# Kernel optimization log

Measured on AMD Instinct MI355X. Metric: run time of the kernel, lower is better.

## Reference

```python
import jax, jax.numpy as jnp
import numpy as np

N_NODES = 50000
N_EDGES = 1_600_000
NUM_GRAPHS = 64
F_NODE = 32
F_EDGE = 16
H = 64
L = 3
BN_EPS = 1e-5


def setup_inputs() -> dict:
    key = jax.random.key(0)
    ks = jax.random.split(key, 20)
    x = jax.random.normal(ks[0], (N_NODES, F_NODE), jnp.float32)
    edge_attr = jax.random.normal(ks[1], (N_EDGES, F_EDGE), jnp.float32)
    edge_index = jax.random.randint(ks[2], (2, N_EDGES), 0, N_NODES, dtype=jnp.int64)
    batch = jnp.sort(jax.random.randint(ks[3], (N_NODES,), 0, NUM_GRAPHS, dtype=jnp.int64))

    def lin(k, fan_in, shape):
        return jax.random.normal(k, shape, jnp.float32) * (1.0 / np.sqrt(fan_in))

    node_W = lin(ks[4], F_NODE, (F_NODE, H));  node_b = jnp.zeros((H,), jnp.float32)
    edge_W = lin(ks[5], F_EDGE, (F_EDGE, H));  edge_b = jnp.zeros((H,), jnp.float32)
    # GINE per-layer MLP: Linear(H, 2H) -> ReLU -> Linear(2H, H)
    W1s = lin(ks[6], H, (L, H, 2 * H));   b1s = jnp.zeros((L, 2 * H), jnp.float32)
    W2s = lin(ks[7], 2 * H, (L, 2 * H, H)); b2s = jnp.zeros((L, H), jnp.float32)
    gammas = jnp.ones((L, H), jnp.float32)
    betas = jnp.zeros((L, H), jnp.float32)
    lin_W = lin(ks[8], H, (H, 1));  lin_b = jnp.zeros((1,), jnp.float32)
    return {
        "x": x, "edge_attr": edge_attr, "edge_index": edge_index, "batch": batch,
        "node_W": node_W, "node_b": node_b, "edge_W": edge_W, "edge_b": edge_b,
        "W1s": W1s, "b1s": b1s, "W2s": W2s, "b2s": b2s,
        "gammas": gammas, "betas": betas, "lin_W": lin_W, "lin_b": lin_b,
    }


def reference(x, edge_attr, edge_index, batch, node_W, node_b, edge_W, edge_b,
              W1s, b1s, W2s, b2s, gammas, betas, lin_W, lin_b):
    # node / edge embeddings
    h = x @ node_W + node_b                  # [N, H]
    e = edge_attr @ edge_W + edge_b          # [E, H]
    src, dst = edge_index[0], edge_index[1]
    for l in range(L):
        # GINEConv (eps=0): m_ij = relu(x_j + e_ij), aggregate sum at target
        m = jax.nn.relu(h[src] + e)                                  # [E, H]
        agg = jax.ops.segment_sum(m, dst, num_segments=N_NODES)     # [N, H]
        z = h + agg
        z = jax.nn.relu(z @ W1s[l] + b1s[l]) @ W2s[l] + b2s[l]       # GINE MLP
        # BatchNorm (training-mode batch stats, biased variance) + ReLU
        mu = jnp.mean(z, axis=0)
        var = jnp.var(z, axis=0)
        h = jax.nn.relu(gammas[l] * (z - mu) * jax.lax.rsqrt(var + BN_EPS) + betas[l])
    # global mean pool per graph
    counts = jax.ops.segment_sum(jnp.ones((N_NODES,), h.dtype), batch, num_segments=NUM_GRAPHS)
    gsum = jax.ops.segment_sum(h, batch, num_segments=NUM_GRAPHS)   # [G, H]
    graph_x = gsum / jnp.maximum(counts, 1.0)[:, None]
    return graph_x @ lin_W + lin_b                                   # [G, 1]
```

## Files before the change

### kernel.cpp

```cpp
#include <hip/hip_runtime.h>

#define NN 50000
#define NE 1600000
#define NG 64
#define HD 64
#define BN_EPS 1e-5f
#define NTILES ((NN + 31) / 32)
#define NBUCK 8
#define NPB 6250
#define NBINS (NBUCK * NN)
#define NEP (NE + 512)
#define SLOTS 3584
#define CHUNK 2000
#define NCHUNK (NBINS / CHUNK)
#define CPB (NCHUNK / NBUCK)

typedef unsigned short ushort_t;
typedef unsigned int uint_t;
typedef __attribute__((ext_vector_type(8))) short bf16x8;
typedef __attribute__((ext_vector_type(4))) float f32x4;

__device__ __forceinline__ float b2f(ushort_t u) {
  union { uint_t i; float f; } v; v.i = ((uint_t)u) << 16; return v.f;
}
__device__ __forceinline__ ushort_t f2b(float f) {
  union { float f; uint_t i; } v; v.f = f;
  uint_t x = v.i;
  return (ushort_t)((x + 0x7fffu + ((x >> 16) & 1u)) >> 16);
}
__device__ __forceinline__ uint_t packsplit(float f) {
  ushort_t hi = f2b(f);
  float r = f - b2f(hi);
  ushort_t lo = f2b(r);
  return (uint_t)hi | ((uint_t)lo << 16);
}
__device__ __forceinline__ float LDF(const void* p, int i, int isb) {
  return isb ? b2f(((const ushort_t*)p)[i]) : ((const float*)p)[i];
}
__device__ __forceinline__ int LDI(const void* p, int i, int is64) {
  return is64 ? ((const int*)p)[2 * i] : ((const int*)p)[i];
}
__device__ __forceinline__ int clampi(int v, int hi) {
  return (v < 0) ? 0 : (v >= hi ? hi - 1 : v);
}

__global__ void detect_k(const uint_t* __restrict__ xw, const uint_t* __restrict__ ew,
                         int* __restrict__ flags) {
  int t = threadIdx.x;
  uint_t w = xw[t];
  uint_t b = (w >> 8) & 0x7fu;
  unsigned long long m1 = __ballot(b >= 0x3au && b <= 0x42u);
  unsigned long long m2 = __ballot(ew[2 * t + 1] == 0u);
  if (t == 0) {
    flags[0] = (__popcll(m1) >= 32) ? 1 : 0;
    flags[1] = (__popcll(m2) >= 56) ? 1 : 0;
  }
}

__global__ void __launch_bounds__(256) node_embed(
    const void* __restrict__ x, const void* __restrict__ W,
    const void* __restrict__ b, float* __restrict__ h, const int* __restrict__ flags) {
  __shared__ float xs[64 * 32];
  int isb = flags[0];
  int t = threadIdx.x;
  int base = blockIdx.x * 64;
  int nodes = NN - base; if (nodes > 64) nodes = 64;
  int idx = t * 8;
  if (idx < nodes * 32) {
    if (isb) {
      const uint4* p = (const uint4*)((const ushort_t*)x + base * 32);
      uint4 u = p[t];
      ushort_t* pu = (ushort_t*)&u;
      #pragma unroll
      for (int q = 0; q < 8; q++) xs[idx + q] = b2f(pu[q]);
    } else {
      const float4* p = (const float4*)((const float*)x + base * 32);
      float4 a = p[2 * t], d = p[2 * t + 1];
      xs[idx + 0] = a.x; xs[idx + 1] = a.y; xs[idx + 2] = a.z; xs[idx + 3] = a.w;
      xs[idx + 4] = d.x; xs[idx + 5] = d.y; xs[idx + 6] = d.z; xs[idx + 7] = d.w;
    }
  }
  int c = t & 63, s0 = t >> 6;
  float w[32];
  #pragma unroll
  for (int k = 0; k < 32; k++) w[k] = LDF(W, k * 64 + c, isb);
  float bc = LDF(b, c, isb);
  __syncthreads();
  #pragma unroll 4
  for (int i = 0; i < 16; i++) {
    int slot = s0 * 16 + i;
    int node = base + slot;
    if (node < NN) {
      float acc = bc;
      #pragma unroll
      for (int k = 0; k < 32; k++) acc += xs[slot * 32 + k] * w[k];
      h[node * 64 + c] = acc;
    }
  }
}

__global__ void __launch_bounds__(256) hist_k(
    const void* __restrict__ eidx, int* __restrict__ hist, const int* __restrict__ flags) {
  int is64 = flags[1];
  int e = blockIdx.x * 256 + threadIdx.x;
  if (e >= NE) return;
  int d = clampi(LDI(eidx, NE + e, is64), NN);
  int s = clampi(LDI(eidx, e, is64), NN);
  int bin = (s / NPB) * NN + d;
  atomicAdd(&hist[bin], 1);
}

__global__ void __launch_bounds__(256) scan_a(
    const int* __restrict__ hist, int* __restrict__ csum) {
  __shared__ int red[256];
  int c = blockIdx.x, t = threadIdx.x;
  int s = 0;
  if (t < 250) {
    const int4* h4 = (const int4*)(hist + c * CHUNK) + t * 2;
    int4 a = h4[0], b = h4[1];
    s = a.x + a.y + a.z + a.w + b.x + b.y + b.z + b.w;
  }
  red[t] = s;
  __syncthreads();
  for (int d = 128; d > 0; d >>= 1) {
    if (t < d) red[t] += red[t + d];
    __syncthreads();
  }
  if (t == 0) csum[c] = red[0];
}

__global__ void __launch_bounds__(256) scan_b(
    const int* __restrict__ csum, int* __restrict__ cbase, int* __restrict__ meta) {
  __shared__ int sc[NCHUNK];
  __shared__ int sT[NBUCK];
  __shared__ int sA[NBUCK + 1];
  int t = threadIdx.x;
  if (t < NCHUNK) sc[t] = csum[t];
  __syncthreads();
  if (t < NBUCK) {
    int T = 0;
    for (int i = 0; i < CPB; i++) T += sc[t * CPB + i];
    sT[t] = T;
  }
  __syncthreads();
  if (t == 0) {
    int a = 0;
    for (int b = 0; b < NBUCK; b++) {
      sA[b] = a;
      meta[b] = a;
      meta[16 + b] = a + sT[b];
      a = (a + sT[b] + 63) & ~63;
    }
    meta[NBUCK] = a;
    sA[NBUCK] = a;
  }
  __syncthreads();
  if (t < NBUCK) {
    int run = sA[t];
    for (int i = 0; i < CPB; i++) { cbase[t * CPB + i] = run; run += sc[t * CPB + i]; }
  }
}

__global__ void __launch_bounds__(256) scan_c(
    const int* __restrict__ hist, const int* __restrict__ cbase,
    int* __restrict__ starts) {
  __shared__ int buf[256];
  int c = blockIdx.x, t = threadIdx.x;
  int4 a = {0, 0, 0, 0}, b = {0, 0, 0, 0};
  int s = 0;
  if (t < 250) {
    const int4* h4 = (const int4*)(hist + c * CHUNK) + t * 2;
    a = h4[0]; b = h4[1];
    s = a.x + a.y + a.z + a.w + b.x + b.y + b.z + b.w;
  }
  buf[t] = s;
  __syncthreads();
  for (int d = 1; d < 256; d <<= 1) {
    int x = (t >= d) ? buf[t - d] : 0;
    __syncthreads();
    buf[t] += x;
    __syncthreads();
  }
  if (t < 250) {
    int run = cbase[c] + buf[t] - s;
    int4 o1, o2;
    o1.x = run; run += a.x;
    o1.y = run; run += a.y;
    o1.z = run; run += a.z;
    o1.w = run; run += a.w;
    o2.x = run; run += b.x;
    o2.y = run; run += b.y;
    o2.z = run; run += b.z;
    o2.w = run; run += b.w;
    int4* s4 = (int4*)(starts + c * CHUNK) + t * 2;
    s4[0] = o1; s4[1] = o2;
  }
}

__global__ void pad_fill(const int* __restrict__ meta, int* __restrict__ perm,
                         int* __restrict__ psrc, int* __restrict__ pdst) {
  int t = threadIdx.x;
  for (int b = 0; b < NBUCK; b++) {
    int re = meta[16 + b], ae = meta[b + 1];
    for (int p = re + t; p < ae; p += 64) {
      perm[p] = 0; psrc[p] = 0; pdst[p] = NN;
    }
  }
}

__global__ void __launch_bounds__(256) scatter_k(
    const void* __restrict__ eidx, int* __restrict__ cursor,
    int* __restrict__ perm, int* __restrict__ psrc, int* __restrict__ pdst,
    const int* __restrict__ flags) {
  int is64 = flags[1];
  int e = blockIdx.x * 256 + threadIdx.x;
  if (e >= NE) return;
  int d = clampi(LDI(eidx, NE + e, is64), NN);
  int s = clampi(LDI(eidx, e, is64), NN);
  int bin = (s / NPB) * NN + d;
  int pos = atomicAdd(&cursor[bin], 1);
  perm[pos] = e;
  psrc[pos] = s;
  pdst[pos] = d;
}

__global__ void __launch_bounds__(256) pack_eattr(
    const void* __restrict__ eattr, const int* __restrict__ perm,
    ushort_t* __restrict__ phi, ushort_t* __restrict__ plo,
    const int* __restrict__ flags, const int* __restrict__ meta) {
  int isb = flags[0];
  int pos = blockIdx.x * 256 + threadIdx.x;
  if (pos >= meta[8]) return;
  int e = perm[pos];
  int tile = pos >> 4, r = pos & 15;
  union U8 { ushort_t s[8]; uint4 u; };
  if (isb) {
    const uint4* p = (const uint4*)((const ushort_t*)eattr + (size_t)e * 16);
    uint4 h0 = p[0], h1 = p[1];
    ((uint4*)phi)[tile * 32 + r] = h0;
    ((uint4*)phi)[tile * 32 + 16 + r] = h1;
  } else {
    const float4* p = (const float4*)((const float*)eattr + (size_t)e * 16);
    U8 hi[2], lo[2];
    #pragma unroll
    for (int q = 0; q < 4; q++) {
      float4 v = p[q];
      float vv[4] = {v.x, v.y, v.z, v.w};
      #pragma unroll
      for (int j = 0; j < 4; j++) {
        int idx = q * 4 + j;
        ushort_t hb = f2b(vv[j]);
        hi[idx >> 3].s[idx & 7] = hb;
        lo[idx >> 3].s[idx & 7] = f2b(vv[j] - b2f(hb));
      }
    }
    ((uint4*)phi)[tile * 32 + r] = hi[0].u;
    ((uint4*)phi)[tile * 32 + 16 + r] = hi[1].u;
    ((uint4*)plo)[tile * 32 + r] = lo[0].u;
    ((uint4*)plo)[tile * 32 + 16 + r] = lo[1].u;
  }
}

__global__ void __launch_bounds__(256) edge_mfma(
    const ushort_t* __restrict__ phi, const ushort_t* __restrict__ plo,
    const int* __restrict__ psrc, const int* __restrict__ pdst,
    const uint4* __restrict__ wfrag, const float* __restrict__ h,
    float* __restrict__ agg, const int* __restrict__ flags,
    const int* __restrict__ meta) {
  __shared__ float es[64 * 68];
  __shared__ int ss[64], sd[64];
  int A[9];
  #pragma unroll
  for (int b = 0; b < 9; b++) A[b] = meta[b];
  int maxcb = 0;
  #pragma unroll
  for (int b = 0; b < NBUCK; b++) {
    int cb = (A[b + 1] - A[b]) >> 6;
    maxcb = cb > maxcb ? cb : maxcb;
  }
  int chunk;
  if (maxcb <= SLOTS) {
    int xcd = blockIdx.x & 7, s = blockIdx.x >> 3;
    if (s >= ((A[xcd + 1] - A[xcd]) >> 6)) return;
    chunk = (A[xcd] >> 6) + s;
  } else {
    chunk = blockIdx.x;
    if (chunk * 64 >= A[8]) return;
  }
  int base = chunk * 64;
  int isb = flags[0];
  int t = threadIdx.x;
  if (t < 64) ss[t] = psrc[base + t];
  else if (t < 128) sd[t - 64] = pdst[base + t - 64];
  int w = t >> 6, lane = t & 63, kg = lane >> 4, cr = lane & 15;
  int tile = chunk * 4 + w;
  union FR { uint4 u; bf16x8 v; };
  FR ahi, alo;
  ahi.u = make_uint4(0u, 0u, 0u, 0u);
  alo.u = ahi.u;
  if (kg < 2) {
    ahi.u = ((const uint4*)phi)[tile * 32 + kg * 16 + cr];
    if (!isb) alo.u = ((const uint4*)plo)[tile * 32 + kg * 16 + cr];
  }
  f32x4 acc[4];
  #pragma unroll
  for (int nt = 0; nt < 4; nt++) acc[nt] = (f32x4){0.f, 0.f, 0.f, 0.f};
  #pragma unroll
  for (int nt = 0; nt < 4; nt++) {
    FR bh; bh.u = wfrag[nt * 64 + lane];
    acc[nt] = __builtin_amdgcn_mfma_f32_16x16x32_bf16(ahi.v, bh.v, acc[nt], 0, 0, 0);
    if (!isb) {
      FR bl; bl.u = wfrag[256 + nt * 64 + lane];
      acc[nt] = __builtin_amdgcn_mfma_f32_16x16x32_bf16(ahi.v, bl.v, acc[nt], 0, 0, 0);
      acc[nt] = __builtin_amdgcn_mfma_f32_16x16x32_bf16(alo.v, bh.v, acc[nt], 0, 0, 0);
    }
  }
  const float* ebias = (const float*)(wfrag + 512);
  #pragma unroll
  for (int nt = 0; nt < 4; nt++) {
    float bv = ebias[nt * 16 + cr];
    #pragma unroll
    for (int r = 0; r < 4; r++)
      es[(w * 16 + kg * 4 + r) * 68 + nt * 16 + cr] = acc[nt][r] + bv;
  }
  __syncthreads();
  int c = lane, s0 = w;
  float hv[16];
  #pragma unroll
  for (int i = 0; i < 16; i++)
    hv[i] = h[(size_t)ss[s0 * 16 + i] * 64 + c];
  float accr = 0.f;
  int cur = -1;
  #pragma unroll
  for (int i = 0; i < 16; i++) {
    int slot = s0 * 16 + i;
    int dn = sd[slot];
    float m = hv[i] + es[slot * 68 + c];
    m = m > 0.f ? m : 0.f;
    if (dn != cur) {
      if (cur >= 0 && cur < NN) atomicAdd(&agg[cur * 64 + c], accr);
      cur = dn; accr = 0.f;
    }
    accr += m;
  }
  if (cur >= 0 && cur < NN) atomicAdd(&agg[cur * 64 + c], accr);
}

__global__ void __launch_bounds__(256) edge_sorted(
    const void* __restrict__ eattr, const int* __restrict__ perm,
    const int* __restrict__ psrc, const int* __restrict__ pdst,
    const void* __restrict__ eW, const void* __restrict__ eb,
    const float* __restrict__ h, float* __restrict__ agg,
    const int* __restrict__ flags, const int* __restrict__ meta) {
  __shared__ float ea[64 * 16];
  __shared__ int ss[64], sd[64];
  int isb = flags[0];
  int t = threadIdx.x;
  int base = blockIdx.x * 64;
  if (base >= meta[8]) return;
  if (t < 64) ss[t] = psrc[base + t];
  else if (t < 128) sd[t - 64] = pdst[base + t - 64];
  {
    int slot = t >> 2, q = t & 3;
    int pe = perm[base + slot];
    if (isb) {
      const uint2* p = (const uint2*)((const ushort_t*)eattr + (size_t)pe * 16 + q * 4);
      uint2 u = *p;
      ea[slot * 16 + q * 4 + 0] = b2f((ushort_t)(u.x & 0xffffu));
      ea[slot * 16 + q * 4 + 1] = b2f((ushort_t)(u.x >> 16));
      ea[slot * 16 + q * 4 + 2] = b2f((ushort_t)(u.y & 0xffffu));
      ea[slot * 16 + q * 4 + 3] = b2f((ushort_t)(u.y >> 16));
    } else {
      const float4* p = (const float4*)((const float*)eattr + (size_t)pe * 16 + q * 4);
      float4 v = *p;
      ea[slot * 16 + q * 4 + 0] = v.x;
      ea[slot * 16 + q * 4 + 1] = v.y;
      ea[slot * 16 + q * 4 + 2] = v.z;
      ea[slot * 16 + q * 4 + 3] = v.w;
    }
  }
  int c = t & 63, s0 = t >> 6;
  float w[16];
  #pragma unroll
  for (int k = 0; k < 16; k++) w[k] = LDF(eW, k * 64 + c, isb);
  float bc = LDF(eb, c, isb);
  __syncthreads();
  float acc = 0.f;
  int cur = -1;
  for (int i = 0; i < 16; i++) {
    int slot = s0 * 16 + i;
    int sn = ss[slot], dn = sd[slot];
    float e = bc;
    #pragma unroll
    for (int k = 0; k < 16; k++) e += ea[slot * 16 + k] * w[k];
    float m = h[sn * 64 + c] + e;
    m = m > 0.f ? m : 0.f;
    if (dn != cur) {
      if (cur >= 0 && cur < NN) atomicAdd(&agg[cur * 64 + c], acc);
      cur = dn; acc = 0.f;
    }
    acc += m;
  }
  if (cur >= 0 && cur < NN) atomicAdd(&agg[cur * 64 + c], acc);
}

__global__ void __launch_bounds__(256) prep_w(
    const void* __restrict__ W1s, const void* __restrict__ W2s,
    const void* __restrict__ eW, const void* __restrict__ eB,
    uint4* __restrict__ wpk, const int* __restrict__ flags) {
  int l = blockIdx.x, t = threadIdx.x, isb = flags[0];
  union U8 { ushort_t s[8]; uint4 u; };
  if (l == 3) {
    uint4* wfrag = wpk + 3 * 4096;
    int nt = t >> 6, lane = t & 63;
    int col = nt * 16 + (lane & 15);
    U8 hi, lo;
    #pragma unroll
    for (int j = 0; j < 8; j++) {
      int k = (lane >> 4) * 8 + j;
      float wf = (k < 16) ? LDF(eW, k * 64 + col, isb) : 0.f;
      ushort_t hb = f2b(wf);
      hi.s[j] = hb;
      lo.s[j] = f2b(wf - b2f(hb));
    }
    wfrag[nt * 64 + lane] = hi.u;
    wfrag[256 + nt * 64 + lane] = lo.u;
    if (t < 64) ((float*)(wfrag + 512))[t] = LDF(eB, t, isb);
    return;
  }
  uint4* w1hi = wpk + (size_t)l * 4096;
  uint4* w1lo = w1hi + 1024;
  uint4* w2hi = w1hi + 2048;
  uint4* w2lo = w1hi + 3072;
  for (int o = t; o < 1024; o += 256) {
    int lane = o & 63, f = (o >> 6) & 7, hh = o >> 9;
    int q = lane >> 4, m = lane & 15;
    {
      int kc = f >> 2, i = f & 3;
      U8 hi, lo;
      #pragma unroll
      for (int j = 0; j < 8; j++) {
        int idx = l * 8192 + (kc * 32 + q * 8 + j) * 128 + (hh * 4 + i) * 16 + m;
        float wf = LDF(W1s, idx, isb);
        ushort_t hb = f2b(wf);
        hi.s[j] = hb;
        lo.s[j] = f2b(wf - b2f(hb));
      }
      w1hi[o] = hi.u;
      w1lo[o] = lo.u;
    }
    {
      int kc = f >> 1, i = f & 1;
      U8 hi, lo;
      #pragma unroll
      for (int j = 0; j < 8; j++) {
        int idx = l * 8192 + (kc * 32 + q * 8 + j) * 64 + (hh * 2 + i) * 16 + m;
        float wf = LDF(W2s, idx, isb);
        ushort_t hb = f2b(wf);
        hi.s[j] = hb;
        lo.s[j] = f2b(wf - b2f(hb));
      }
      w2hi[o] = hi.u;
      w2lo[o] = lo.u;
    }
  }
}

__global__ void __launch_bounds__(256) mlp_mfma(
    const float* __restrict__ h, const float* agg,
    const uint4* __restrict__ wpk, const void* __restrict__ b1s,
    const void* __restrict__ b2s,
    float* z2out, float* __restrict__ bnsum, const int* __restrict__ flags, int layer) {
  __shared__ uint_t zs[32 * 65];
  __shared__ uint_t a1s[32 * 129];
  int isb = flags[0];
  int t = threadIdx.x;
  int w = t >> 6, lane = t & 63, q = lane >> 4, m = lane & 15;
  int mt = w & 1;
  int hh = w >> 1;
  int ng1 = hh * 4;
  int ng2 = hh * 2;
  int b1off = layer * 128, b2off = layer * 64;
  const uint4* w1hi = wpk + (size_t)layer * 4096;
  const uint4* w1lo = w1hi + 1024;
  const uint4* w2hi = w1hi + 2048;
  const uint4* w2lo = w1hi + 3072;

  union FR { uint4 u; bf16x8 v; };
  FR w1f[4][2], w2f[2][4];
  #pragma unroll
  for (int kc = 0; kc < 2; kc++)
    #pragma unroll
    for (int i = 0; i < 4; i++)
      w1f[i][kc].u = w1hi[(hh * 8 + kc * 4 + i) * 64 + lane];
  #pragma unroll
  for (int kc = 0; kc < 4; kc++)
    #pragma unroll
    for (int i = 0; i < 2; i++)
      w2f[i][kc].u = w2hi[(hh * 8 + kc * 2 + i) * 64 + lane];

  float b1v[4], b2v[2];
  #pragma unroll
  for (int i = 0; i < 4; i++) b1v[i] = LDF(b1s, b1off + (ng1 + i) * 16 + m, isb);
  #pragma unroll
  for (int i = 0; i < 2; i++) b2v[i] = LDF(b2s, b2off + (ng2 + i) * 16 + m, isb);

  int srow = t >> 3, scol = (t & 7) * 8;
  float ps[2] = {0.f, 0.f}, pq[2] = {0.f, 0.f};

  for (int tile = blockIdx.x; tile < NTILES; tile += gridDim.x) {
    int base = tile * 32;
    __syncthreads();
    {
      int gr = base + srow;
      if (gr < NN) {
        const float4* hp = (const float4*)(h + (size_t)gr * 64 + scol);
        const float4* ap = (const float4*)(agg + (size_t)gr * 64 + scol);
        float4 h0 = hp[0], h1 = hp[1], a0 = ap[0], a1 = ap[1];
        zs[srow * 65 + scol + 0] = packsplit(h0.x + a0.x);
        zs[srow * 65 + scol + 1] = packsplit(h0.y + a0.y);
        zs[srow * 65 + scol + 2] = packsplit(h0.z + a0.z);
        zs[srow * 65 + scol + 3] = packsplit(h0.w + a0.w);
        zs[srow * 65 + scol + 4] = packsplit(h1.x + a1.x);
        zs[srow * 65 + scol + 5] = packsplit(h1.y + a1.y);
        zs[srow * 65 + scol + 6] = packsplit(h1.z + a1.z);
        zs[srow * 65 + scol + 7] = packsplit(h1.w + a1.w);
      } else {
        #pragma unroll
        for (int jj = 0; jj < 8; jj++) zs[srow * 65 + scol + jj] = 0;
      }
    }
    __syncthreads();
    f32x4 acc1[4];
    #pragma unroll
    for (int i = 0; i < 4; i++) acc1[i] = (f32x4){0.f, 0.f, 0.f, 0.f};
    #pragma unroll
    for (int kc = 0; kc < 2; kc++) {
      int ab = (mt * 16 + m) * 65 + kc * 32 + q * 8;
      bf16x8 ahi, alo;
      #pragma unroll
      for (int j = 0; j < 8; j++) {
        uint_t u = zs[ab + j];
        ahi[j] = (short)(u & 0xffffu);
        alo[j] = (short)(u >> 16);
      }
      #pragma unroll
      for (int i = 0; i < 4; i++) {
        acc1[i] = __builtin_amdgcn_mfma_f32_16x16x32_bf16(ahi, w1f[i][kc].v, acc1[i], 0, 0, 0);
        acc1[i] = __builtin_amdgcn_mfma_f32_16x16x32_bf16(alo, w1f[i][kc].v, acc1[i], 0, 0, 0);
        if (!isb) {
          FR bl;
          bl.u = w1lo[(hh * 8 + kc * 4 + i) * 64 + lane];
          acc1[i] = __builtin_amdgcn_mfma_f32_16x16x32_bf16(ahi, bl.v, acc1[i], 0, 0, 0);
        }
      }
    }
    #pragma unroll
    for (int i = 0; i < 4; i++) {
      #pragma unroll
      for (int r = 0; r < 4; r++) {
        float v = acc1[i][r] + b1v[i];
        v = v > 0.f ? v : 0.f;
        a1s[(mt * 16 + q * 4 + r) * 129 + (ng1 + i) * 16 + m] = packsplit(v);
      }
    }
    __syncthreads();
    f32x4 acc2[2];
    #pragma unroll
    for (int i = 0; i < 2; i++) acc2[i] = (f32x4){0.f, 0.f, 0.f, 0.f};
    #pragma unroll
    for (int kc = 0; kc < 4; kc++) {
      int ab = (mt * 16 + m) * 129 + kc * 32 + q * 8;
      bf16x8 ahi, alo;
      #pragma unroll
      for (int j = 0; j < 8; j++) {
        uint_t u = a1s[ab + j];
        ahi[j] = (short)(u & 0xffffu);
        alo[j] = (short)(u >> 16);
      }
      #pragma unroll
      for (int i = 0; i < 2; i++) {
        acc2[i] = __builtin_amdgcn_mfma_f32_16x16x32_bf16(ahi, w2f[i][kc].v, acc2[i], 0, 0, 0);
        acc2[i] = __builtin_amdgcn_mfma_f32_16x16x32_bf16(alo, w2f[i][kc].v, acc2[i], 0, 0, 0);
        if (!isb) {
          FR bl;
          bl.u = w2lo[(hh * 8 + kc * 2 + i) * 64 + lane];
          acc2[i] = __builtin_amdgcn_mfma_f32_16x16x32_bf16(ahi, bl.v, acc2[i], 0, 0, 0);
        }
      }
    }
    #pragma unroll
    for (int i = 0; i < 2; i++) {
      int col = (ng2 + i) * 16 + m;
      #pragma unroll
      for (int r = 0; r < 4; r++) {
        int gr = base + mt * 16 + q * 4 + r;
        if (gr < NN) {
          float v = acc2[i][r] + b2v[i];
          z2out[(size_t)gr * 64 + col] = v;
          ps[i] += v; pq[i] += v * v;
        }
      }
    }
  }
  __syncthreads();
  float* red = (float*)zs;
  if (t < 128) red[t] = 0.f;
  __syncthreads();
  #pragma unroll
  for (int i = 0; i < 2; i++) {
    int col = (ng2 + i) * 16 + m;
    atomicAdd(&red[col], ps[i]);
    atomicAdd(&red[64 + col], pq[i]);
  }
  __syncthreads();
  if (t < 128) atomicAdd(&bnsum[t], red[t]);
}

__global__ void bn_fin(const float* __restrict__ bnsum, const void* __restrict__ gammas,
                       const void* __restrict__ betas, float* __restrict__ scsh,
                       const int* __restrict__ flags, int layer) {
  int c = threadIdx.x;
  int isb = flags[0];
  float inv_n = 1.0f / (float)NN;
  float mu = bnsum[c] * inv_n;
  float var = bnsum[64 + c] * inv_n - mu * mu;
  var = var > 0.f ? var : 0.f;
  float sc = LDF(gammas, layer * 64 + c, isb) * rsqrtf(var + BN_EPS);
  scsh[c] = sc;
  scsh[64 + c] = LDF(betas, layer * 64 + c, isb) - mu * sc;
}

__global__ void __launch_bounds__(256) bn_apply(
    const float* __restrict__ z2, const float* __restrict__ scsh, float* __restrict__ h) {
  int t = blockIdx.x * 256 + threadIdx.x;
  if (t < NN * 16) {
    float4 z = ((const float4*)z2)[t];
    int c4 = t & 15;
    float4 sc = ((const float4*)scsh)[c4];
    float4 sh = ((const float4*)(scsh + 64))[c4];
    float4 r;
    r.x = fmaxf(z.x * sc.x + sh.x, 0.f);
    r.y = fmaxf(z.y * sc.y + sh.y, 0.f);
    r.z = fmaxf(z.z * sc.z + sh.z, 0.f);
    r.w = fmaxf(z.w * sc.w + sh.w, 0.f);
    ((float4*)h)[t] = r;
  }
}

__global__ void __launch_bounds__(256) find_bounds(
    const void* __restrict__ batch, int* __restrict__ bounds, const int* __restrict__ flags) {
  int is64 = flags[1];
  int i = blockIdx.x * 256 + threadIdx.x;
  if (i >= NN) return;
  int cur = clampi(LDI(batch, i, is64), NG);
  if (i == 0) {
    for (int g = 0; g <= cur; g++) bounds[g] = 0;
  } else {
    int prev = clampi(LDI(batch, i - 1, is64), NG);
    for (int g = prev + 1; g <= cur; g++) bounds[g] = i;
  }
  if (i == NN - 1) {
    for (int g = cur + 1; g <= NG; g++) bounds[g] = NN;
  }
}

__global__ void __launch_bounds__(256) pool_final(
    const float* __restrict__ h, const int* __restrict__ bounds,
    const void* __restrict__ linW, const void* __restrict__ linB,
    float* __restrict__ out, const int* __restrict__ flags) {
  __shared__ float red[4][64];
  int isb = flags[0];
  int g = blockIdx.x;
  int t = threadIdx.x, c = t & 63, w = t >> 6;
  int s = bounds[g], e = bounds[g + 1];
  float acc = 0.f;
  for (int i = s + w; i < e; i += 4) acc += h[i * 64 + c];
  red[w][c] = acc;
  __syncthreads();
  if (t < 64) {
    float v = red[0][c] + red[1][c] + red[2][c] + red[3][c];
    float cnt = (float)(e - s); if (cnt < 1.f) cnt = 1.f;
    v = (v / cnt) * LDF(linW, c, isb);
    #pragma unroll
    for (int m = 32; m >= 1; m >>= 1) v += __shfl_xor(v, m, 64);
    if (c == 0) out[g] = v + LDF(linB, 0, isb);
  }
}

extern "C" void kernel_launch(void* const* d_in, const int* in_sizes, int n_in,
                              void* d_out, int out_size, void* d_ws, size_t ws_size,
                              hipStream_t stream) {
  const void* x     = d_in[0];
  const void* eattr = d_in[1];
  const void* eidx  = d_in[2];
  const void* batch = d_in[3];
  const void* nodeW = d_in[4];
  const void* nodeB = d_in[5];
  const void* edgeW = d_in[6];
  const void* edgeB = d_in[7];
  const void* W1s   = d_in[8];
  const void* b1s   = d_in[9];
  const void* W2s   = d_in[10];
  const void* b2s   = d_in[11];
  const void* gam   = d_in[12];
  const void* bet   = d_in[13];
  const void* linW  = d_in[14];
  const void* linB  = d_in[15];
  float* out = (float*)d_out;

  int*   flags  = (int*)d_ws;
  int*   meta   = flags + 16;
  float* h      = (float*)(meta + 48);
  float* agg    = h + (size_t)NN * HD;
  float* bnsum  = agg + (size_t)NN * HD;
  float* scsh   = bnsum + 128;
  int*   bounds = (int*)(scsh + 128);
  int*   csum   = bounds + 80;
  int*   cbase  = csum + NCHUNK;
  int*   offs   = cbase + NCHUNK;
  int*   cursor = offs + NBINS;
  int*   perm   = cursor + NBINS;
  int*   psrc   = perm + NEP;
  int*   pdst   = psrc + NEP;

  size_t base_words = 64ull + 2ull * NN * HD + 128 + 128 + 80
                    + 2ull * NCHUNK + 2ull * NBINS + 3ull * NEP;
  size_t wpk_words_start = (base_words + 3ull) & ~3ull;
  size_t wpk_words = (3ull * 4096 + 528) * 4;
  size_t needed = (wpk_words_start + wpk_words) * 4ull;
  if (ws_size < needed) return;
  uint4* wpk = (uint4*)((float*)d_ws + wpk_words_start);
  uint4* wfrag = wpk + 3ull * 4096;
  size_t z2_start = wpk_words_start + wpk_words;
  float* z2sep = (float*)d_ws + z2_start;
  int have_z2 = ws_size >= (z2_start + (size_t)NN * HD) * 4ull;
  float* z2 = have_z2 ? z2sep : agg;
  size_t pat_start = z2_start + (size_t)NN * HD;
  size_t pat_words = (size_t)NEP * 8;
  int have_pat = have_z2 && (ws_size >= (pat_start + 2ull * pat_words) * 4ull);
  ushort_t* phi = (ushort_t*)((float*)d_ws + pat_start);
  ushort_t* plo = (ushort_t*)((float*)d_ws + pat_start + pat_words);

  detect_k<<<1, 64, 0, stream>>>((const uint_t*)x, (const uint_t*)eidx, flags);
  prep_w<<<4, 256, 0, stream>>>(W1s, W2s, edgeW, edgeB, wpk, flags);
  node_embed<<<(NN + 63) / 64, 256, 0, stream>>>(x, nodeW, nodeB, h, flags);

  hipMemsetAsync(offs, 0, (size_t)NBINS * sizeof(int), stream);
  hist_k<<<NE / 256, 256, 0, stream>>>(eidx, offs, flags);
  scan_a<<<NCHUNK, 256, 0, stream>>>(offs, csum);
  scan_b<<<1, 256, 0, stream>>>(csum, cbase, meta);
  scan_c<<<NCHUNK, 256, 0, stream>>>(offs, cbase, cursor);
  pad_fill<<<1, 64, 0, stream>>>(meta, perm, psrc, pdst);
  scatter_k<<<NE / 256, 256, 0, stream>>>(eidx, cursor, perm, psrc, pdst, flags);
  if (have_pat)
    pack_eattr<<<NEP / 256, 256, 0, stream>>>(eattr, perm, phi, plo, flags, meta);

  for (int l = 0; l < 3; l++) {
    hipMemsetAsync(agg, 0, (size_t)NN * HD * sizeof(float), stream);
    if (have_pat)
      edge_mfma<<<8 * SLOTS, 256, 0, stream>>>(phi, plo, psrc, pdst, wfrag, h, agg, flags, meta);
    else
      edge_sorted<<<NEP / 64, 256, 0, stream>>>(eattr, perm, psrc, pdst, edgeW, edgeB, h, agg, flags, meta);
    hipMemsetAsync(bnsum, 0, 128 * sizeof(int), stream);
    mlp_mfma<<<784, 256, 0, stream>>>(h, agg, wpk, b1s, b2s, z2, bnsum, flags, l);
    bn_fin<<<1, 64, 0, stream>>>(bnsum, gam, bet, scsh, flags, l);
    bn_apply<<<3125, 256, 0, stream>>>(z2, scsh, h);
  }
  find_bounds<<<(NN + 255) / 256, 256, 0, stream>>>(batch, bounds, flags);
  pool_final<<<NG, 256, 0, stream>>>(h, bounds, linW, linB, out, flags);
}
```

Baseline: 948.8 us.

## Bin edges by destination block then source bucket for 64 sub-buckets

Measured after the change: 995.8 us. 4.9% more time.

```diff
diff --git a/kernel.cpp b/kernel.cpp
--- a/kernel.cpp
+++ b/kernel.cpp
@@ -8,12 +8,10 @@
 #define NTILES ((NN + 31) / 32)
 #define NBUCK 8
 #define NPB 6250
-#define NBINS (NBUCK * NN)
-#define NEP (NE + 512)
+#define NSB 64
+#define NBINS (NSB * NPB)
+#define NEP (NE + 4096)
 #define SLOTS 3584
-#define CHUNK 2000
-#define NCHUNK (NBINS / CHUNK)
-#define CPB (NCHUNK / NBUCK)
 
 typedef unsigned short ushort_t;
 typedef unsigned int uint_t;
@@ -106,19 +104,20 @@
   if (e >= NE) return;
   int d = clampi(LDI(eidx, NE + e, is64), NN);
   int s = clampi(LDI(eidx, e, is64), NN);
-  int bin = (s / NPB) * NN + d;
+  int bd = d / NPB, bs = s / NPB;
+  int bin = (bd * 8 + bs) * NPB + (d - bd * NPB);
   atomicAdd(&hist[bin], 1);
 }
 
 __global__ void __launch_bounds__(256) scan_a(
     const int* __restrict__ hist, int* __restrict__ csum) {
   __shared__ int red[256];
-  int c = blockIdx.x, t = threadIdx.x;
+  int sb = blockIdx.x, t = threadIdx.x;
   int s = 0;
   if (t < 250) {
-    const int4* h4 = (const int4*)(hist + c * CHUNK) + t * 2;
-    int4 a = h4[0], b = h4[1];
-    s = a.x + a.y + a.z + a.w + b.x + b.y + b.z + b.w;
+    const int* p = hist + sb * NPB + t * 25;
+    #pragma unroll 5
+    for (int i = 0; i < 25; i++) s += p[i];
   }
   red[t] = s;
   __syncthreads();
@@ -126,52 +125,35 @@
     if (t < d) red[t] += red[t + d];
     __syncthreads();
   }
-  if (t == 0) csum[c] = red[0];
-}
-
-__global__ void __launch_bounds__(256) scan_b(
-    const int* __restrict__ csum, int* __restrict__ cbase, int* __restrict__ meta) {
-  __shared__ int sc[NCHUNK];
-  __shared__ int sT[NBUCK];
-  __shared__ int sA[NBUCK + 1];
-  int t = threadIdx.x;
-  if (t < NCHUNK) sc[t] = csum[t];
-  __syncthreads();
-  if (t < NBUCK) {
-    int T = 0;
-    for (int i = 0; i < CPB; i++) T += sc[t * CPB + i];
-    sT[t] = T;
-  }
-  __syncthreads();
-  if (t == 0) {
+  if (t == 0) csum[sb] = red[0];
+}
+
+__global__ void scan_b(const int* __restrict__ csum, int* __restrict__ meta) {
+  if (threadIdx.x == 0) {
     int a = 0;
-    for (int b = 0; b < NBUCK; b++) {
-      sA[b] = a;
-      meta[b] = a;
-      meta[16 + b] = a + sT[b];
-      a = (a + sT[b] + 63) & ~63;
-    }
-    meta[NBUCK] = a;
-    sA[NBUCK] = a;
-  }
-  __syncthreads();
-  if (t < NBUCK) {
-    int run = sA[t];
-    for (int i = 0; i < CPB; i++) { cbase[t * CPB + i] = run; run += sc[t * CPB + i]; }
+    for (int sb = 0; sb < NSB; sb++) {
+      meta[sb] = a;
+      int T = csum[sb];
+      meta[128 + sb] = a + T;
+      a = (a + T + 63) & ~63;
+    }
+    meta[64] = a;
+    for (int x = 0; x < 8; x++) meta[96 + x] = meta[x * 8];
+    meta[96 + 8] = a;
   }
 }
 
 __global__ void __launch_bounds__(256) scan_c(
-    const int* __restrict__ hist, const int* __restrict__ cbase,
+    const int* __restrict__ hist, const int* __restrict__ meta,
     int* __restrict__ starts) {
   __shared__ int buf[256];
-  int c = blockIdx.x, t = threadIdx.x;
-  int4 a = {0, 0, 0, 0}, b = {0, 0, 0, 0};
+  int sb = blockIdx.x, t = threadIdx.x;
+  int loc[25];
   int s = 0;
   if (t < 250) {
-    const int4* h4 = (const int4*)(hist + c * CHUNK) + t * 2;
-    a = h4[0]; b = h4[1];
-    s = a.x + a.y + a.z + a.w + b.x + b.y + b.z + b.w;
+    const int* p = hist + sb * NPB + t * 25;
+    #pragma unroll 5
+    for (int i = 0; i < 25; i++) { loc[i] = p[i]; s += loc[i]; }
   }
   buf[t] = s;
   __syncthreads();
@@ -182,26 +164,19 @@
     __syncthreads();
   }
   if (t < 250) {
-    int run = cbase[c] + buf[t] - s;
-    int4 o1, o2;
-    o1.x = run; run += a.x;
-    o1.y = run; run += a.y;
-    o1.z = run; run += a.z;
-    o1.w = run; run += a.w;
-    o2.x = run; run += b.x;
-    o2.y = run; run += b.y;
-    o2.z = run; run += b.z;
-    o2.w = run; run += b.w;
-    int4* s4 = (int4*)(starts + c * CHUNK) + t * 2;
-    s4[0] = o1; s4[1] = o2;
+    int run = meta[sb] + buf[t] - s;
+    int* q = starts + sb * NPB + t * 25;
+    #pragma unroll 5
+    for (int i = 0; i < 25; i++) { q[i] = run; run += loc[i]; }
   }
 }
 
 __global__ void pad_fill(const int* __restrict__ meta, int* __restrict__ perm,
                          int* __restrict__ psrc, int* __restrict__ pdst) {
   int t = threadIdx.x;
-  for (int b = 0; b < NBUCK; b++) {
-    int re = meta[16 + b], ae = meta[b + 1];
+  for (int sb = 0; sb < NSB; sb++) {
+    int re = meta[128 + sb];
+    int ae = (sb < NSB - 1) ? meta[sb + 1] : meta[64];
     for (int p = re + t; p < ae; p += 64) {
       perm[p] = 0; psrc[p] = 0; pdst[p] = NN;
     }
@@ -217,7 +192,8 @@
   if (e >= NE) return;
   int d = clampi(LDI(eidx, NE + e, is64), NN);
   int s = clampi(LDI(eidx, e, is64), NN);
-  int bin = (s / NPB) * NN + d;
+  int bd = d / NPB, bs = s / NPB;
+  int bin = (bd * 8 + bs) * NPB + (d - bd * NPB);
   int pos = atomicAdd(&cursor[bin], 1);
   perm[pos] = e;
   psrc[pos] = s;
@@ -230,7 +206,7 @@
     const int* __restrict__ flags, const int* __restrict__ meta) {
   int isb = flags[0];
   int pos = blockIdx.x * 256 + threadIdx.x;
-  if (pos >= meta[8]) return;
+  if (pos >= meta[64]) return;
   int e = perm[pos];
   int tile = pos >> 4, r = pos & 15;
   union U8 { ushort_t s[8]; uint4 u; };
@@ -271,10 +247,10 @@
   __shared__ int ss[64], sd[64];
   int A[9];
   #pragma unroll
-  for (int b = 0; b < 9; b++) A[b] = meta[b];
+  for (int b = 0; b < 9; b++) A[b] = meta[96 + b];
   int maxcb = 0;
   #pragma unroll
-  for (int b = 0; b < NBUCK; b++) {
+  for (int b = 0; b < 8; b++) {
     int cb = (A[b + 1] - A[b]) >> 6;
     maxcb = cb > maxcb ? cb : maxcb;
   }
@@ -357,7 +333,7 @@
   int isb = flags[0];
   int t = threadIdx.x;
   int base = blockIdx.x * 64;
-  if (base >= meta[8]) return;
+  if (base >= meta[64]) return;
   if (t < 64) ss[t] = psrc[base + t];
   else if (t < 128) sd[t - 64] = pdst[base + t - 64];
   {
@@ -711,21 +687,20 @@
 
   int*   flags  = (int*)d_ws;
   int*   meta   = flags + 16;
-  float* h      = (float*)(meta + 48);
+  float* h      = (float*)(meta + 192);
   float* agg    = h + (size_t)NN * HD;
   float* bnsum  = agg + (size_t)NN * HD;
   float* scsh   = bnsum + 128;
   int*   bounds = (int*)(scsh + 128);
   int*   csum   = bounds + 80;
-  int*   cbase  = csum + NCHUNK;
-  int*   offs   = cbase + NCHUNK;
+  int*   offs   = csum + NSB;
   int*   cursor = offs + NBINS;
   int*   perm   = cursor + NBINS;
   int*   psrc   = perm + NEP;
   int*   pdst   = psrc + NEP;
 
-  size_t base_words = 64ull + 2ull * NN * HD + 128 + 128 + 80
-                    + 2ull * NCHUNK + 2ull * NBINS + 3ull * NEP;
+  size_t base_words = 16ull + 192 + 2ull * NN * HD + 128 + 128 + 80
+                    + NSB + 2ull * NBINS + 3ull * NEP;
   size_t wpk_words_start = (base_words + 3ull) & ~3ull;
   size_t wpk_words = (3ull * 4096 + 528) * 4;
   size_t needed = (wpk_words_start + wpk_words) * 4ull;
@@ -748,9 +723,9 @@
 
   hipMemsetAsync(offs, 0, (size_t)NBINS * sizeof(int), stream);
   hist_k<<<NE / 256, 256, 0, stream>>>(eidx, offs, flags);
-  scan_a<<<NCHUNK, 256, 0, stream>>>(offs, csum);
-  scan_b<<<1, 256, 0, stream>>>(csum, cbase, meta);
-  scan_c<<<NCHUNK, 256, 0, stream>>>(offs, cbase, cursor);
+  scan_a<<<NSB, 256, 0, stream>>>(offs, csum);
+  scan_b<<<1, 64, 0, stream>>>(csum, meta);
+  scan_c<<<NSB, 256, 0, stream>>>(offs, meta, cursor);
   pad_fill<<<1, 64, 0, stream>>>(meta, perm, psrc, pdst);
   scatter_k<<<NE / 256, 256, 0, stream>>>(eidx, cursor, perm, psrc, pdst, flags);
   if (have_pat)
```

## Process 128 edges per block with per-wave LDS and shuffle-based indices

Applied to the files above, without the earlier changes.

New measurement: 912.3 us. 1.04x faster.

```diff
diff --git a/kernel.cpp b/kernel.cpp
--- a/kernel.cpp
+++ b/kernel.cpp
@@ -9,8 +9,8 @@
 #define NBUCK 8
 #define NPB 6250
 #define NBINS (NBUCK * NN)
-#define NEP (NE + 512)
-#define SLOTS 3584
+#define NEP (NE + 2048)
+#define SLOTS 1792
 #define CHUNK 2000
 #define NCHUNK (NBINS / CHUNK)
 #define CPB (NCHUNK / NBUCK)
@@ -149,7 +149,7 @@
       sA[b] = a;
       meta[b] = a;
       meta[16 + b] = a + sT[b];
-      a = (a + sT[b] + 63) & ~63;
+      a = (a + sT[b] + 127) & ~127;
     }
     meta[NBUCK] = a;
     sA[NBUCK] = a;
@@ -267,81 +267,94 @@
     const uint4* __restrict__ wfrag, const float* __restrict__ h,
     float* __restrict__ agg, const int* __restrict__ flags,
     const int* __restrict__ meta) {
-  __shared__ float es[64 * 68];
-  __shared__ int ss[64], sd[64];
+  __shared__ float es[4][16 * 68];
   int A[9];
   #pragma unroll
   for (int b = 0; b < 9; b++) A[b] = meta[b];
   int maxcb = 0;
   #pragma unroll
   for (int b = 0; b < NBUCK; b++) {
-    int cb = (A[b + 1] - A[b]) >> 6;
+    int cb = (A[b + 1] - A[b]) >> 7;
     maxcb = cb > maxcb ? cb : maxcb;
   }
   int chunk;
   if (maxcb <= SLOTS) {
     int xcd = blockIdx.x & 7, s = blockIdx.x >> 3;
-    if (s >= ((A[xcd + 1] - A[xcd]) >> 6)) return;
-    chunk = (A[xcd] >> 6) + s;
+    if (s >= ((A[xcd + 1] - A[xcd]) >> 7)) return;
+    chunk = (A[xcd] >> 7) + s;
   } else {
     chunk = blockIdx.x;
-    if (chunk * 64 >= A[8]) return;
-  }
-  int base = chunk * 64;
+    if (chunk * 128 >= A[8]) return;
+  }
   int isb = flags[0];
   int t = threadIdx.x;
-  if (t < 64) ss[t] = psrc[base + t];
-  else if (t < 128) sd[t - 64] = pdst[base + t - 64];
   int w = t >> 6, lane = t & 63, kg = lane >> 4, cr = lane & 15;
-  int tile = chunk * 4 + w;
+  int ebase = chunk * 128 + w * 32;
+  int li = lane & 31;
+  int vidx = (lane < 32) ? psrc[ebase + li] : pdst[ebase + li];
   union FR { uint4 u; bf16x8 v; };
-  FR ahi, alo;
-  ahi.u = make_uint4(0u, 0u, 0u, 0u);
-  alo.u = ahi.u;
-  if (kg < 2) {
-    ahi.u = ((const uint4*)phi)[tile * 32 + kg * 16 + cr];
-    if (!isb) alo.u = ((const uint4*)plo)[tile * 32 + kg * 16 + cr];
-  }
-  f32x4 acc[4];
-  #pragma unroll
-  for (int nt = 0; nt < 4; nt++) acc[nt] = (f32x4){0.f, 0.f, 0.f, 0.f};
-  #pragma unroll
-  for (int nt = 0; nt < 4; nt++) {
-    FR bh; bh.u = wfrag[nt * 64 + lane];
-    acc[nt] = __builtin_amdgcn_mfma_f32_16x16x32_bf16(ahi.v, bh.v, acc[nt], 0, 0, 0);
-    if (!isb) {
-      FR bl; bl.u = wfrag[256 + nt * 64 + lane];
-      acc[nt] = __builtin_amdgcn_mfma_f32_16x16x32_bf16(ahi.v, bl.v, acc[nt], 0, 0, 0);
-      acc[nt] = __builtin_amdgcn_mfma_f32_16x16x32_bf16(alo.v, bh.v, acc[nt], 0, 0, 0);
-    }
+  FR bh[4], bl[4];
+  #pragma unroll
+  for (int nt = 0; nt < 4; nt++) bh[nt].u = wfrag[nt * 64 + lane];
+  if (!isb) {
+    #pragma unroll
+    for (int nt = 0; nt < 4; nt++) bl[nt].u = wfrag[256 + nt * 64 + lane];
   }
   const float* ebias = (const float*)(wfrag + 512);
-  #pragma unroll
-  for (int nt = 0; nt < 4; nt++) {
-    float bv = ebias[nt * 16 + cr];
-    #pragma unroll
-    for (int r = 0; r < 4; r++)
-      es[(w * 16 + kg * 4 + r) * 68 + nt * 16 + cr] = acc[nt][r] + bv;
-  }
-  __syncthreads();
-  int c = lane, s0 = w;
-  float hv[16];
-  #pragma unroll
-  for (int i = 0; i < 16; i++)
-    hv[i] = h[(size_t)ss[s0 * 16 + i] * 64 + c];
+  float bv[4];
+  #pragma unroll
+  for (int nt = 0; nt < 4; nt++) bv[nt] = ebias[nt * 16 + cr];
+  int c = lane;
   float accr = 0.f;
   int cur = -1;
   #pragma unroll
-  for (int i = 0; i < 16; i++) {
-    int slot = s0 * 16 + i;
-    int dn = sd[slot];
-    float m = hv[i] + es[slot * 68 + c];
-    m = m > 0.f ? m : 0.f;
-    if (dn != cur) {
-      if (cur >= 0 && cur < NN) atomicAdd(&agg[cur * 64 + c], accr);
-      cur = dn; accr = 0.f;
-    }
-    accr += m;
+  for (int st = 0; st < 2; st++) {
+    int tile = chunk * 8 + w * 2 + st;
+    FR ahi, alo;
+    ahi.u = make_uint4(0u, 0u, 0u, 0u);
+    alo.u = ahi.u;
+    if (kg < 2) {
+      ahi.u = ((const uint4*)phi)[tile * 32 + kg * 16 + cr];
+      if (!isb) alo.u = ((const uint4*)plo)[tile * 32 + kg * 16 + cr];
+    }
+    f32x4 acc[4];
+    #pragma unroll
+    for (int nt = 0; nt < 4; nt++) acc[nt] = (f32x4){0.f, 0.f, 0.f, 0.f};
+    #pragma unroll
+    for (int nt = 0; nt < 4; nt++) {
+      acc[nt] = __builtin_amdgcn_mfma_f32_16x16x32_bf16(ahi.v, bh[nt].v, acc[nt], 0, 0, 0);
+      if (!isb) {
+        acc[nt] = __builtin_amdgcn_mfma_f32_16x16x32_bf16(ahi.v, bl[nt].v, acc[nt], 0, 0, 0);
+        acc[nt] = __builtin_amdgcn_mfma_f32_16x16x32_bf16(alo.v, bh[nt].v, acc[nt], 0, 0, 0);
+      }
+    }
+    asm volatile("s_waitcnt lgkmcnt(0)" ::: "memory");
+    __builtin_amdgcn_sched_barrier(0);
+    #pragma unroll
+    for (int nt = 0; nt < 4; nt++) {
+      #pragma unroll
+      for (int r = 0; r < 4; r++)
+        es[w][(kg * 4 + r) * 68 + nt * 16 + cr] = acc[nt][r] + bv[nt];
+    }
+    asm volatile("s_waitcnt lgkmcnt(0)" ::: "memory");
+    __builtin_amdgcn_sched_barrier(0);
+    float hv[16];
+    #pragma unroll
+    for (int i = 0; i < 16; i++) {
+      int sn = __shfl(vidx, st * 16 + i, 64);
+      hv[i] = h[(size_t)sn * 64 + c];
+    }
+    #pragma unroll
+    for (int i = 0; i < 16; i++) {
+      int dn = __shfl(vidx, 32 + st * 16 + i, 64);
+      float m = hv[i] + es[w][i * 68 + c];
+      m = m > 0.f ? m : 0.f;
+      if (dn != cur) {
+        if (cur >= 0 && cur < NN) atomicAdd(&agg[cur * 64 + c], accr);
+        cur = dn; accr = 0.f;
+      }
+      accr += m;
+    }
   }
   if (cur >= 0 && cur < NN) atomicAdd(&agg[cur * 64 + c], accr);
 }
```
